# Kernel optimization log

Hardware: AMD Instinct MI355X
Metric: run time of the kernel (lower is better)

Reference implementation:

```python
import jax, jax.numpy as jnp
import numpy as np

B, N, D, H, DK, NREL, TOPK = 32, 49, 512, 8, 64, 14, 14
EPS = 1e-5
SCALE = float(1.0 / np.sqrt(DK))


def _linear(x, W, b):
    return x @ W + b


def _ln(x, g, b):
    m = jnp.mean(x, -1, keepdims=True)
    v = jnp.var(x, -1, keepdims=True)
    return (x - m) * jax.lax.rsqrt(v + EPS) * g + b


def setup_inputs() -> dict:
    key = jax.random.key(0)
    ks = jax.random.split(key, 24)

    def rn(k, shape, s=0.03):
        return (jax.random.normal(k, shape) * s).astype(jnp.float32)

    inp = {}
    inp['queries'] = jax.random.normal(ks[0], (B, N, D), jnp.float32)
    inp['keys'] = jax.random.normal(ks[1], (B, N, D), jnp.float32)
    inp['values'] = jax.random.normal(ks[2], (B, N, D), jnp.float32)
    inp['Wq'] = rn(ks[3], (D, H * DK)); inp['bq'] = jnp.zeros((H * DK,), jnp.float32)
    inp['Wk'] = rn(ks[4], (D, H * DK)); inp['bk'] = jnp.zeros((H * DK,), jnp.float32)
    inp['Wv'] = rn(ks[5], (D, H * DK)); inp['bv'] = jnp.zeros((H * DK,), jnp.float32)
    inp['Wo'] = rn(ks[6], (H * DK, D)); inp['bo'] = jnp.zeros((D,), jnp.float32)
    inp['rel_embed'] = rn(ks[7], (NREL, DK), 0.5)
    inp['Wproj'] = rn(ks[8], (DK, D)); inp['bproj'] = jnp.zeros((D,), jnp.float32)
    inp['Wgate'] = rn(ks[9], (D, 1)); inp['bgate'] = jnp.zeros((1,), jnp.float32)
    inp['Wc1'] = rn(ks[10], (2 * D, 256)); inp['bc1'] = jnp.zeros((256,), jnp.float32)
    inp['gc'] = jnp.ones((256,), jnp.float32); inp['bcln'] = jnp.zeros((256,), jnp.float32)
    inp['Wc2'] = rn(ks[11], (256, NREL)); inp['bc2'] = jnp.zeros((NREL,), jnp.float32)
    inp['Wr1'] = rn(ks[12], (2 * D, D)); inp['br1'] = jnp.zeros((D,), jnp.float32)
    inp['gr'] = jnp.ones((D,), jnp.float32); inp['brln'] = jnp.zeros((D,), jnp.float32)
    inp['Wr2'] = rn(ks[13], (D, D)); inp['br2'] = jnp.zeros((D,), jnp.float32)
    inp['convW'] = rn(ks[14], (D, D, 3, 3)); inp['convb'] = jnp.zeros((D,), jnp.float32)
    return inp


def reference(queries, keys, values, Wq, bq, Wk, bk, Wv, bv, Wo, bo,
              rel_embed, Wproj, bproj, Wgate, bgate,
              Wc1, bc1, gc, bcln, Wc2, bc2,
              Wr1, br1, gr, brln, Wr2, br2, convW, convb):
    Bsz, nq, _ = queries.shape
    # spatial_net: conv3x3 -> BatchNorm2d(affine=False, training stats) -> ReLU
    x = queries.transpose(0, 2, 1).reshape(Bsz, D, 7, 7)
    h = jax.lax.conv_general_dilated(x, convW, (1, 1), ((1, 1), (1, 1)),
                                     dimension_numbers=('NCHW', 'OIHW', 'NCHW'))
    h = h + convb[None, :, None, None]
    mu = jnp.mean(h, (0, 2, 3), keepdims=True)
    var = jnp.var(h, (0, 2, 3), keepdims=True)
    h = jax.nn.relu((h - mu) * jax.lax.rsqrt(var + EPS))
    xs = h.reshape(Bsz, D, nq).transpose(0, 2, 1)  # [B,49,D]
    eq = xs + queries
    ek = xs + keys
    ev = xs + values
    nk = ek.shape[1]
    # multi-head projections
    q = _linear(eq, Wq, bq).reshape(Bsz, nq, H, DK).transpose(0, 2, 1, 3)
    k = _linear(ek, Wk, bk).reshape(Bsz, nk, H, DK).transpose(0, 2, 1, 3)
    v = _linear(ev, Wv, bv).reshape(Bsz, nk, H, DK).transpose(0, 2, 1, 3)
    att = jnp.einsum('bhqd,bhkd->bhqk', q, k) * SCALE
    # pairwise relation features [B,nq,nk,2D]
    pair = jnp.concatenate([
        jnp.broadcast_to(eq[:, :, None, :], (Bsz, nq, nk, D)),
        jnp.broadcast_to(ek[:, None, :, :], (Bsz, nq, nk, D))], -1)
    logits = _linear(jax.nn.relu(_ln(_linear(pair, Wc1, bc1), gc, bcln)), Wc2, bc2)
    probs = jax.nn.softmax(logits, -1)
    tp, ti = jax.lax.top_k(probs, TOPK)
    tp = tp / (jnp.sum(tp, -1, keepdims=True) + 1e-8)
    rel_emb = jnp.sum(tp[..., None] * rel_embed[ti], -2)  # [B,nq,nk,DK]
    proj = _linear(rel_emb, Wproj, bproj)
    rf = _linear(jax.nn.relu(_ln(_linear(pair, Wr1, br1), gr, brln)), Wr2, br2)
    gate = jax.nn.sigmoid(_linear(rf + proj, Wgate, bgate))[..., 0]  # [B,nq,nk]
    enh = att * (1.0 + gate[:, None, :, :])
    w = jax.nn.softmax(enh, -1)
    out = jnp.einsum('bhqk,bhkd->bhqd', w, v).transpose(0, 2, 1, 3).reshape(Bsz, nq, H * DK)
    return _linear(out, Wo, bo)
```

## Files before the change

### kernel.cpp

```cpp
#include <hip/hip_runtime.h>
#include <math.h>

typedef _Float16 f16;
typedef _Float16 f16x2 __attribute__((ext_vector_type(2)));
typedef _Float16 f16x8 __attribute__((ext_vector_type(8)));
typedef float f32x4 __attribute__((ext_vector_type(4)));

static constexpr int Mrows = 1568;
static constexpr int NPAIR = 76832;
static constexpr float SCALEC = 0.125f;
#define EPSV 1e-5f

__device__ inline float wsum(float v) {
#pragma unroll
  for (int m = 32; m >= 1; m >>= 1) v += __shfl_xor(v, m, 64);
  return v;
}
__device__ inline float wmax(float v) {
#pragma unroll
  for (int m = 32; m >= 1; m >>= 1) v = fmaxf(v, __shfl_xor(v, m, 64));
  return v;
}
__device__ inline void gld16(const void* g, void* l) {
  __builtin_amdgcn_global_load_lds((const __attribute__((address_space(1))) void*)g,
                                   (__attribute__((address_space(3))) void*)l, 16, 0, 0);
}
__device__ inline f16x2 H2(unsigned u) { return __builtin_bit_cast(f16x2, u); }
__device__ inline unsigned U32(f16x2 h) { return __builtin_bit_cast(unsigned, h); }
__device__ inline f16x2 pk2(float a, float b) {
  return __builtin_bit_cast(f16x2, __builtin_amdgcn_cvt_pkrtz(a, b));
}
__device__ inline float qsum(float v) {
  v += __shfl_xor(v, 1, 64);
  v += __shfl_xor(v, 2, 64);
  return v;
}

__global__ __launch_bounds__(256) void prep(const float* __restrict__ queries,
                                            const float* __restrict__ convW,
                                            float* __restrict__ h,
                                            f16* __restrict__ Qp,
                                            f16* __restrict__ Wtb) {
  int bx = blockIdx.x;
  int tid = threadIdx.x;
  if (bx < 784) {
    ((float4*)h)[bx * 256 + tid] = make_float4(0.f, 0.f, 0.f, 0.f);
  } else if (bx < 784 + 5184) {
    int idx = (bx - 784) * 256 + tid;
    int c = idx & 511;
    int iijj = (idx >> 9) % 81;
    int b = idx / (81 * 512);
    int ii = iijj / 9, jj = iijj % 9;
    float v = 0.f;
    if (ii >= 1 && ii <= 7 && jj >= 1 && jj <= 7)
      v = queries[(((size_t)(b * 49 + (ii - 1) * 7 + (jj - 1))) << 9) + c];
    Qp[idx] = (f16)v;
  } else {
    int idx = (bx - 5968) * 256 + tid;
    int o = idx >> 9, c = idx & 511;
    const float* s = convW + (size_t)o * 4608 + c * 9;
    f16* d = Wtb + (size_t)o * 4608 + c;
#pragma unroll
    for (int t = 0; t < 9; t++) d[t * 512] = (f16)s[t];
  }
}

__global__ __launch_bounds__(256) void smalls_kernel(
    const float* __restrict__ Wproj, const float* __restrict__ Wgate,
    const float* __restrict__ rel_embed, const float* __restrict__ bproj,
    const float* __restrict__ br2, const float* __restrict__ bgate,
    const float* __restrict__ Wr2, float* __restrict__ crel,
    float* __restrict__ wrg, float* __restrict__ cconst) {
  int tid = threadIdx.x;
  if (blockIdx.x == 0) {
    __shared__ float pg[64];
    if (tid < 64) {
      float s = 0.f;
      for (int d = 0; d < 512; d++) s += Wproj[tid * 512 + d] * Wgate[d];
      pg[tid] = s;
    }
    __syncthreads();
    if (tid < 14) {
      float s = 0.f;
      for (int dk = 0; dk < 64; dk++) s += rel_embed[tid * 64 + dk] * pg[dk];
      crel[tid] = s;
    }
    if (tid == 64) {
      float s = 0.f;
      for (int d = 0; d < 512; d++) s += (bproj[d] + br2[d]) * Wgate[d];
      cconst[0] = s + bgate[0];
    }
  } else {
    int d = (blockIdx.x - 1) * 256 + tid;
    float s = 0.f;
    for (int d2 = 0; d2 < 512; d2++) s += Wr2[(size_t)d * 512 + d2] * Wgate[d2];
    wrg[d] = s;
  }
}

struct TJobs { const float* src[8]; f16* dst[8]; int cols[8]; };
__global__ __launch_bounds__(256) void transpose_w(TJobs tj) {
  int z = blockIdx.z;
  int cols = tj.cols[z];
  int n0 = blockIdx.x * 32;
  if (n0 >= cols) return;
  int k0 = blockIdx.y * 32;
  const float* src = tj.src[z];
  f16* dst = tj.dst[z];
  __shared__ float tile[32][33];
  int tid = threadIdx.x;
  int c = tid & 31, r0 = tid >> 5;
#pragma unroll
  for (int i = 0; i < 4; i++) {
    int r = r0 + i * 8;
    tile[r][c] = src[(size_t)(k0 + r) * cols + n0 + c];
  }
  __syncthreads();
#pragma unroll
  for (int i = 0; i < 4; i++) {
    int r = r0 + i * 8;
    dst[(size_t)(n0 + r) * 512 + k0 + c] = (f16)tile[c][r];
  }
}

struct T2Jobs { const float* src[4]; unsigned* dst[4]; int C[4]; };
__global__ __launch_bounds__(256) void t2h(T2Jobs tj) {
  int z = blockIdx.z;
  int C = tj.C[z];
  int c0 = blockIdx.x * 32;
  if (c0 >= C) return;
  int r0 = blockIdx.y * 32;
  const float* src = tj.src[z];
  unsigned* dst = tj.dst[z];
  __shared__ float tile[32][33];
  int t = threadIdx.x;
  int cc = t & 31, rr = t >> 5;
#pragma unroll
  for (int i = 0; i < 4; i++)
    tile[cc][rr + i * 8] = src[(size_t)(r0 + rr + i * 8) * C + c0 + cc];
  __syncthreads();
  int r = t & 31, cp = t >> 5;
#pragma unroll
  for (int i = 0; i < 2; i++) {
    int c = cp + i * 8;
    f16x2 p = pk2(tile[2 * c][r], tile[2 * c + 1][r]);
    dst[(size_t)((c0 >> 1) + c) * 1568 + r0 + r] = U32(p);
  }
}

__global__ __launch_bounds__(256) void conv_mfma(const f16* __restrict__ Qp,
                                                 const f16* __restrict__ Wtb,
                                                 float* __restrict__ h) {
  __shared__ f16 As2[2048];
  __shared__ f16 Bs2[2048];
  int tid = threadIdx.x;
  int n0 = blockIdx.x * 64;
  int m0 = blockIdx.y * 64;
  int kb = blockIdx.z * 576;
  int lane = tid & 63, wv = tid >> 6;
  int kq = (tid >> 4) & 3, mm = tid & 15;
  int rowA = m0 + wv * 16 + mm;
  if (rowA > Mrows - 1) rowA = Mrows - 1;
  int b = rowA / 49, p = rowA % 49;
  int pi = p / 7, pj = p % 7;
  const f16* qbase = Qp + (size_t)b * 81 * 512 + kq * 8;
  int rowB = n0 + wv * 16 + mm;
  const f16* bSrc = Wtb + (size_t)rowB * 4608 + kq * 8 + kb;
  f16* aDst = &As2[wv * 512];
  f16* bDst = &Bs2[wv * 512];
  f32x4 acc[4];
#pragma unroll
  for (int i = 0; i < 4; i++) acc[i] = (f32x4){0.f, 0.f, 0.f, 0.f};
  for (int s = 0; s < 18; s++) {
    int k0 = kb + s * 32;
    int t = k0 >> 9, c0 = k0 & 511;
    int ti = t / 3, tj = t - ti * 3;
    const f16* aSrc = qbase + (size_t)((pi + ti) * 9 + (pj + tj)) * 512 + c0;
    gld16(aSrc, aDst);
    gld16(bSrc + s * 32, bDst);
    __syncthreads();
    f16x8 a = *(const f16x8*)&As2[(wv << 9) + (lane << 3)];
#pragma unroll
    for (int nb = 0; nb < 4; nb++) {
      f16x8 bf = *(const f16x8*)&Bs2[(nb << 9) + (lane << 3)];
      acc[nb] = __builtin_amdgcn_mfma_f32_16x16x32_f16(a, bf, acc[nb], 0, 0, 0);
    }
    __syncthreads();
  }
  int r0 = m0 + wv * 16 + ((lane >> 4) << 2);
  int cw = lane & 15;
#pragma unroll
  for (int nb = 0; nb < 4; nb++) {
    int col = n0 + nb * 16 + cw;
#pragma unroll
    for (int r = 0; r < 4; r++) {
      int row = r0 + r;
      if (row < Mrows) atomicAdd(&h[(size_t)row * 512 + col], acc[nb][r]);
    }
  }
}

__global__ __launch_bounds__(256) void bn_stats(const float* __restrict__ h,
                                                float* __restrict__ mu,
                                                float* __restrict__ rsg) {
  int c = blockIdx.x;
  int tid = threadIdx.x;
  float s = 0.f, ss = 0.f;
  for (int r = tid; r < Mrows; r += 256) {
    float v = h[(size_t)r * 512 + c];
    s += v;
    ss += v * v;
  }
  s = wsum(s);
  ss = wsum(ss);
  __shared__ float r1[4], r2[4];
  int wave = tid >> 6, lane = tid & 63;
  if (lane == 0) { r1[wave] = s; r2[wave] = ss; }
  __syncthreads();
  if (tid == 0) {
    float S = r1[0] + r1[1] + r1[2] + r1[3];
    float SS = r2[0] + r2[1] + r2[2] + r2[3];
    float m = S / (float)Mrows;
    float var = SS / (float)Mrows - m * m;
    mu[c] = m;
    rsg[c] = rsqrtf(var + EPSV);
  }
}

__global__ __launch_bounds__(256) void fuse_xs(
    const float* __restrict__ h, const float* __restrict__ mu,
    const float* __restrict__ rsg, const float* __restrict__ Q,
    const float* __restrict__ Kin, const float* __restrict__ Vin,
    f16* __restrict__ eqh, f16* __restrict__ ekh, f16* __restrict__ evh) {
  int i = blockIdx.x * 256 + threadIdx.x;
  int c = i & 511;
  float xs = fmaxf((h[i] - mu[c]) * rsg[c], 0.f);
  eqh[i] = (f16)(xs + Q[i]);
  ekh[i] = (f16)(xs + Kin[i]);
  evh[i] = (f16)(xs + Vin[i]);
}

struct MJobs { const f16* A[7]; const f16* BT[7]; const float* bias[7]; float* C[7]; int N[7]; };
__global__ __launch_bounds__(256) void gemm_mf(MJobs jb) {
  int z = blockIdx.z;
  int N = jb.N[z];
  int n0 = blockIdx.x * 64;
  if (n0 >= N) return;
  int m0 = blockIdx.y * 64;
  const f16* A = jb.A[z];
  const f16* BT = jb.BT[z];
  __shared__ f16 As2[2048];
  __shared__ f16 Bs2[2048];
  int tid = threadIdx.x, lane = tid & 63, wv = tid >> 6;
  int kq = (tid >> 4) & 3, mm = tid & 15;
  int rowA = m0 + wv * 16 + mm;
  if (rowA > Mrows - 1) rowA = Mrows - 1;
  const f16* aSrc = A + (size_t)rowA * 512 + kq * 8;
  int rowB = n0 + wv * 16 + mm;
  const f16* bSrc = BT + (size_t)rowB * 512 + kq * 8;
  f16* aDst = &As2[wv * 512];
  f16* bDst = &Bs2[wv * 512];
  f32x4 acc[4];
#pragma unroll
  for (int i = 0; i < 4; i++) acc[i] = (f32x4){0.f, 0.f, 0.f, 0.f};
  for (int s = 0; s < 16; s++) {
    gld16(aSrc + s * 32, aDst);
    gld16(bSrc + s * 32, bDst);
    __syncthreads();
    f16x8 a = *(const f16x8*)&As2[(wv << 9) + (lane << 3)];
#pragma unroll
    for (int nb = 0; nb < 4; nb++) {
      f16x8 bf = *(const f16x8*)&Bs2[(nb << 9) + (lane << 3)];
      acc[nb] = __builtin_amdgcn_mfma_f32_16x16x32_f16(a, bf, acc[nb], 0, 0, 0);
    }
    __syncthreads();
  }
  const float* bias = jb.bias[z];
  float* C = jb.C[z];
  int r0 = m0 + wv * 16 + ((lane >> 4) << 2);
  int cw = lane & 15;
#pragma unroll
  for (int nb = 0; nb < 4; nb++) {
    int col = n0 + nb * 16 + cw;
    float bv = bias ? bias[col] : 0.f;
#pragma unroll
    for (int r = 0; r < 4; r++) {
      int row = r0 + r;
      if (row < Mrows) C[(size_t)row * N + col] = acc[nb][r] + bv;
    }
  }
}

__global__ __launch_bounds__(256) void pair_gate(
    const unsigned* __restrict__ CqT, const unsigned* __restrict__ CkT,
    const unsigned* __restrict__ RqT, const unsigned* __restrict__ RkT,
    const float* __restrict__ Wc2, const float* __restrict__ bc2,
    const float* __restrict__ gc, const float* __restrict__ bcln,
    const float* __restrict__ gr, const float* __restrict__ brln,
    const float* __restrict__ crel, const float* __restrict__ wrg,
    const float* __restrict__ cconstp, float* __restrict__ gfac) {
  __shared__ uint4 sTC[512];
  __shared__ uint4 sTR[256];
  __shared__ float scl[14], sb2[14];
  int tid = threadIdx.x;
  if (tid < 128) {
    int dd = tid;
    unsigned w[16];
    w[0] = U32(pk2(gc[2 * dd], gc[2 * dd + 1]));
    w[1] = U32(pk2(bcln[2 * dd], bcln[2 * dd + 1]));
#pragma unroll
    for (int r = 0; r < 14; r++)
      w[2 + r] = U32(pk2(Wc2[(2 * dd) * 14 + r], Wc2[(2 * dd + 1) * 14 + r]));
#pragma unroll
    for (int j = 0; j < 4; j++)
      sTC[dd * 4 + j] = make_uint4(w[4 * j], w[4 * j + 1], w[4 * j + 2], w[4 * j + 3]);
  }
  {
    int dd = tid;
    sTR[dd] = make_uint4(U32(pk2(gr[2 * dd], gr[2 * dd + 1])),
                         U32(pk2(brln[2 * dd], brln[2 * dd + 1])),
                         U32(pk2(wrg[2 * dd], wrg[2 * dd + 1])), 0u);
  }
  if (tid < 14) { scl[tid] = crel[tid]; sb2[tid] = bc2[tid]; }
  __syncthreads();

  int gidx = blockIdx.x * 256 + tid;
  int pid = gidx >> 2;
  int sub = gidx & 3;
  bool valid = pid < NPAIR;
  int pc = valid ? pid : NPAIR - 1;
  int b = pc / 2401;
  int r2 = pc % 2401;
  int q = r2 / 49, k = r2 % 49;
  int rowq = b * 49 + q, rowk = b * 49 + k;
  const f16x2 one2 = {(f16)1.f, (f16)1.f};
  const f16x2 zero2 = {(f16)0.f, (f16)0.f};

  float s1;
  {
    unsigned zc[32];
    const unsigned* cq = CqT + (size_t)sub * 1568 + rowq;
    const unsigned* ck = CkT + (size_t)sub * 1568 + rowk;
    float s = 0.f, ss = 0.f;
#pragma unroll
    for (int j = 0; j < 32; j++) {
      f16x2 z2 = H2(cq[(size_t)j * 4 * 1568]) + H2(ck[(size_t)j * 4 * 1568]);
      zc[j] = U32(z2);
      s = __builtin_amdgcn_fdot2(z2, one2, s, false);
      ss = __builtin_amdgcn_fdot2(z2, z2, ss, false);
    }
    s = qsum(s);
    ss = qsum(ss);
    float mC = s * (1.f / 256.f);
    float var = ss * (1.f / 256.f) - mC * mC;
    float rsC = rsqrtf(var + EPSV);
    f16x2 nm2 = pk2(-mC, -mC);
    f16x2 rs2 = pk2(rsC, rsC);

    float lg[14];
#pragma unroll
    for (int r = 0; r < 14; r++) lg[r] = 0.f;
#pragma unroll
    for (int j = 0; j < 32; j++) {
      int dd = 4 * j + sub;
      uint4 t0 = sTC[dd * 4 + 0];
      uint4 t1 = sTC[dd * 4 + 1];
      uint4 t2 = sTC[dd * 4 + 2];
      uint4 t3 = sTC[dd * 4 + 3];
      f16x2 z2 = H2(zc[j]);
      f16x2 u2 = (z2 + nm2) * rs2;
      f16x2 h2 = __builtin_elementwise_max(u2 * H2(t0.x) + H2(t0.y), zero2);
      lg[0] = __builtin_amdgcn_fdot2(h2, H2(t0.z), lg[0], false);
      lg[1] = __builtin_amdgcn_fdot2(h2, H2(t0.w), lg[1], false);
      lg[2] = __builtin_amdgcn_fdot2(h2, H2(t1.x), lg[2], false);
      lg[3] = __builtin_amdgcn_fdot2(h2, H2(t1.y), lg[3], false);
      lg[4] = __builtin_amdgcn_fdot2(h2, H2(t1.z), lg[4], false);
      lg[5] = __builtin_amdgcn_fdot2(h2, H2(t1.w), lg[5], false);
      lg[6] = __builtin_amdgcn_fdot2(h2, H2(t2.x), lg[6], false);
      lg[7] = __builtin_amdgcn_fdot2(h2, H2(t2.y), lg[7], false);
      lg[8] = __builtin_amdgcn_fdot2(h2, H2(t2.z), lg[8], false);
      lg[9] = __builtin_amdgcn_fdot2(h2, H2(t2.w), lg[9], false);
      lg[10] = __builtin_amdgcn_fdot2(h2, H2(t3.x), lg[10], false);
      lg[11] = __builtin_amdgcn_fdot2(h2, H2(t3.y), lg[11], false);
      lg[12] = __builtin_amdgcn_fdot2(h2, H2(t3.z), lg[12], false);
      lg[13] = __builtin_amdgcn_fdot2(h2, H2(t3.w), lg[13], false);
    }
#pragma unroll
    for (int r = 0; r < 14; r++) lg[r] = qsum(lg[r]) + sb2[r];

    float mx = lg[0];
#pragma unroll
    for (int r = 1; r < 14; r++) mx = fmaxf(mx, lg[r]);
    float se = 0.f, sc = 0.f;
#pragma unroll
    for (int r = 0; r < 14; r++) {
      float e = __expf(lg[r] - mx);
      se += e;
      sc += e * scl[r];
    }
    s1 = sc / (se * (1.f + 1e-8f));
  }

  float s2v;
  {
    unsigned zr[64];
    const unsigned* rq = RqT + (size_t)sub * 1568 + rowq;
    const unsigned* rk = RkT + (size_t)sub * 1568 + rowk;
    float sR = 0.f, ssR = 0.f;
#pragma unroll
    for (int j = 0; j < 64; j++) {
      f16x2 z2 = H2(rq[(size_t)j * 4 * 1568]) + H2(rk[(size_t)j * 4 * 1568]);
      zr[j] = U32(z2);
      sR = __builtin_amdgcn_fdot2(z2, one2, sR, false);
      ssR = __builtin_amdgcn_fdot2(z2, z2, ssR, false);
    }
    sR = qsum(sR);
    ssR = qsum(ssR);
    float mR = sR * (1.f / 512.f);
    float varR = ssR * (1.f / 512.f) - mR * mR;
    float rsR = rsqrtf(varR + EPSV);
    f16x2 nmR2 = pk2(-mR, -mR);
    f16x2 rsR2 = pk2(rsR, rsR);

    float acc = 0.f;
#pragma unroll
    for (int j = 0; j < 64; j++) {
      int dd = 4 * j + sub;
      uint4 tr = sTR[dd];
      f16x2 z2 = H2(zr[j]);
      f16x2 u2 = (z2 + nmR2) * rsR2;
      f16x2 h2 = __builtin_elementwise_max(u2 * H2(tr.x) + H2(tr.y), zero2);
      acc = __builtin_amdgcn_fdot2(h2, H2(tr.z), acc, false);
    }
    s2v = qsum(acc);
  }

  float gin = s1 + s2v + cconstp[0];
  float gate = 1.f / (1.f + __expf(-gin));
  if (valid && sub == 0) gfac[pid] = 1.f + gate;
}

__global__ __launch_bounds__(256) void attn(const float* __restrict__ qb,
                                            const float* __restrict__ kb,
                                            const float* __restrict__ vb,
                                            const float* __restrict__ gfac,
                                            f16* __restrict__ aoh) {
  int b = blockIdx.x >> 3, h = blockIdx.x & 7;
  __shared__ float Kh[64][65];
  __shared__ float Vh[49][65];
  __shared__ float G[2401];
  int tid = threadIdx.x;
  for (int i = tid; i < 49 * 64; i += 256) {
    int k = i >> 6, d = i & 63;
    size_t off = (((size_t)(b * 49 + k)) << 9) + h * 64 + d;
    Kh[k][d] = kb[off];
    Vh[k][d] = vb[off];
  }
  for (int i = tid; i < 15 * 64; i += 256) {
    Kh[49 + (i >> 6)][i & 63] = 0.f;
  }
  for (int i = tid; i < 2401; i += 256) G[i] = gfac[b * 2401 + i];
  __syncthreads();
  int wave = tid >> 6, lane = tid & 63;
  for (int q = wave; q < 49; q += 4) {
    float qv = qb[(((size_t)(b * 49 + q)) << 9) + h * 64 + lane];
    float dot = 0.f;
#pragma unroll
    for (int d = 0; d < 64; d++) dot += __shfl(qv, d, 64) * Kh[lane][d];
    float enh = (lane < 49) ? dot * SCALEC * G[q * 49 + lane] : -1e30f;
    float mxv = wmax(enh);
    float e = (lane < 49) ? __expf(enh - mxv) : 0.f;
    float ssum = wsum(e);
    float w = e / ssum;
    float out = 0.f;
#pragma unroll
    for (int k = 0; k < 49; k++) out += __shfl(w, k, 64) * Vh[k][lane];
    aoh[(((size_t)(b * 49 + q)) << 9) + h * 64 + lane] = (f16)out;
  }
}

extern "C" void kernel_launch(void* const* d_in, const int* in_sizes, int n_in,
                              void* d_out, int out_size, void* d_ws, size_t ws_size,
                              hipStream_t stream) {
  const float* queries = (const float*)d_in[0];
  const float* keys = (const float*)d_in[1];
  const float* values = (const float*)d_in[2];
  const float* Wq = (const float*)d_in[3];
  const float* bq = (const float*)d_in[4];
  const float* Wk = (const float*)d_in[5];
  const float* bk = (const float*)d_in[6];
  const float* Wv = (const float*)d_in[7];
  const float* bv = (const float*)d_in[8];
  const float* Wo = (const float*)d_in[9];
  const float* bo = (const float*)d_in[10];
  const float* rel_embed = (const float*)d_in[11];
  const float* Wproj = (const float*)d_in[12];
  const float* bproj = (const float*)d_in[13];
  const float* Wgate = (const float*)d_in[14];
  const float* bgate = (const float*)d_in[15];
  const float* Wc1 = (const float*)d_in[16];
  const float* bc1 = (const float*)d_in[17];
  const float* gc = (const float*)d_in[18];
  const float* bcln = (const float*)d_in[19];
  const float* Wc2 = (const float*)d_in[20];
  const float* bc2 = (const float*)d_in[21];
  const float* Wr1 = (const float*)d_in[22];
  const float* br1 = (const float*)d_in[23];
  const float* gr = (const float*)d_in[24];
  const float* brln = (const float*)d_in[25];
  const float* Wr2 = (const float*)d_in[26];
  const float* br2 = (const float*)d_in[27];
  const float* convW = (const float*)d_in[28];

  float* W = (float*)d_ws;
  size_t o = 0;
  f16* Qp = (f16*)(W + o); o += 663552;
  f16* Wtb = (f16*)(W + o); o += 1179648;
  f16* WqT = (f16*)(W + o); o += 131072;
  f16* WkT = (f16*)(W + o); o += 131072;
  f16* WvT = (f16*)(W + o); o += 131072;
  f16* WoT = (f16*)(W + o); o += 131072;
  f16* Wc1aT = (f16*)(W + o); o += 65536;
  f16* Wc1bT = (f16*)(W + o); o += 65536;
  f16* Wr1aT = (f16*)(W + o); o += 131072;
  f16* Wr1bT = (f16*)(W + o); o += 131072;
  float* hbuf = W + o; o += 802816;
  f16* eqh = (f16*)(W + o); o += 401408;
  f16* ekh = (f16*)(W + o); o += 401408;
  f16* evh = (f16*)(W + o); o += 401408;
  float* qbuf = W + o; o += 802816;
  float* kbuf = W + o; o += 802816;
  float* vbuf = W + o; o += 802816;
  float* Cqw = W + o; o += 401408;
  float* Ckw = W + o; o += 401408;
  float* Rqw = W + o; o += 802816;
  float* Rkw = W + o; o += 802816;
  f16* aoh = (f16*)(W + o); o += 200704;
  float* gf = W + o; o += 76832;
  float* mu = W + o; o += 512;
  float* rsg = W + o; o += 512;
  float* crel = W + o; o += 16;
  float* wrg = W + o; o += 512;
  float* ccst = W + o; o += 16;
  unsigned* CqT2 = (unsigned*)(W + o); o += 200704;
  unsigned* CkT2 = (unsigned*)(W + o); o += 200704;
  unsigned* RqT2 = (unsigned*)(W + o); o += 401408;
  unsigned* RkT2 = (unsigned*)(W + o); o += 401408;

  hipLaunchKernelGGL(prep, dim3(784 + 5184 + 1024), dim3(256), 0, stream,
                     queries, convW, hbuf, Qp, Wtb);
  hipLaunchKernelGGL(smalls_kernel, dim3(3), dim3(256), 0, stream, Wproj, Wgate,
                     rel_embed, bproj, br2, bgate, Wr2, crel, wrg, ccst);

  TJobs tj;
  tj.src[0] = Wq;  tj.dst[0] = WqT;  tj.cols[0] = 512;
  tj.src[1] = Wk;  tj.dst[1] = WkT;  tj.cols[1] = 512;
  tj.src[2] = Wv;  tj.dst[2] = WvT;  tj.cols[2] = 512;
  tj.src[3] = Wo;  tj.dst[3] = WoT;  tj.cols[3] = 512;
  tj.src[4] = Wc1;             tj.dst[4] = Wc1aT; tj.cols[4] = 256;
  tj.src[5] = Wc1 + 512 * 256; tj.dst[5] = Wc1bT; tj.cols[5] = 256;
  tj.src[6] = Wr1;             tj.dst[6] = Wr1aT; tj.cols[6] = 512;
  tj.src[7] = Wr1 + 512 * 512; tj.dst[7] = Wr1bT; tj.cols[7] = 512;
  hipLaunchKernelGGL(transpose_w, dim3(16, 16, 8), dim3(256), 0, stream, tj);

  hipLaunchKernelGGL(conv_mfma, dim3(8, 25, 8), dim3(256), 0, stream, Qp, Wtb, hbuf);
  hipLaunchKernelGGL(bn_stats, dim3(512), dim3(256), 0, stream, hbuf, mu, rsg);
  hipLaunchKernelGGL(fuse_xs, dim3(3136), dim3(256), 0, stream, hbuf, mu, rsg,
                     queries, keys, values, eqh, ekh, evh);

  MJobs jb;
  jb.A[0] = eqh; jb.BT[0] = WqT;   jb.bias[0] = bq;      jb.C[0] = qbuf; jb.N[0] = 512;
  jb.A[1] = ekh; jb.BT[1] = WkT;   jb.bias[1] = bk;      jb.C[1] = kbuf; jb.N[1] = 512;
  jb.A[2] = evh; jb.BT[2] = WvT;   jb.bias[2] = bv;      jb.C[2] = vbuf; jb.N[2] = 512;
  jb.A[3] = eqh; jb.BT[3] = Wc1aT; jb.bias[3] = bc1;     jb.C[3] = Cqw;  jb.N[3] = 256;
  jb.A[4] = ekh; jb.BT[4] = Wc1bT; jb.bias[4] = nullptr; jb.C[4] = Ckw;  jb.N[4] = 256;
  jb.A[5] = eqh; jb.BT[5] = Wr1aT; jb.bias[5] = br1;     jb.C[5] = Rqw;  jb.N[5] = 512;
  jb.A[6] = ekh; jb.BT[6] = Wr1bT; jb.bias[6] = nullptr; jb.C[6] = Rkw;  jb.N[6] = 512;
  hipLaunchKernelGGL(gemm_mf, dim3(8, 25, 7), dim3(256), 0, stream, jb);

  T2Jobs t2;
  t2.src[0] = Cqw; t2.dst[0] = CqT2; t2.C[0] = 256;
  t2.src[1] = Ckw; t2.dst[1] = CkT2; t2.C[1] = 256;
  t2.src[2] = Rqw; t2.dst[2] = RqT2; t2.C[2] = 512;
  t2.src[3] = Rkw; t2.dst[3] = RkT2; t2.C[3] = 512;
  hipLaunchKernelGGL(t2h, dim3(16, 49, 4), dim3(256), 0, stream, t2);

  hipLaunchKernelGGL(pair_gate, dim3((NPAIR * 4 + 255) / 256), dim3(256), 0, stream,
                     CqT2, CkT2, RqT2, RkT2, Wc2, bc2, gc, bcln, gr, brln, crel,
                     wrg, ccst, gf);
  hipLaunchKernelGGL(attn, dim3(256), dim3(256), 0, stream, qbuf, kbuf, vbuf, gf, aoh);

  MJobs j2;
  j2.A[0] = aoh; j2.BT[0] = WoT; j2.bias[0] = bo; j2.C[0] = (float*)d_out; j2.N[0] = 512;
  for (int z = 1; z < 7; z++) {
    j2.A[z] = nullptr; j2.BT[z] = nullptr; j2.bias[z] = nullptr; j2.C[z] = nullptr; j2.N[z] = 0;
  }
  hipLaunchKernelGGL(gemm_mf, dim3(8, 25, 1), dim3(256), 0, stream, j2);
}
```

Baseline: 358.2 us.

## Decompose pairwise LayerNorm stats into row sums plus per-batch Gram matmuls

The pairwise LayerNorm mean and variance over (Cq+Ck) are now computed algebraically from per-row sums, per-row sums of squares, and a 2*Cq·Ck cross term. The cross term comes from a new per-batch MFMA Gram kernel, and the row sums come from a separate kernel. This removes the first pass over the pair features in pair_gate and the large register buffers that pass needed, lowering register pressure. In exchange it adds two kernels, f16 copies of the GEMM outputs, and the one-pass variance formula with f16-rounded cross terms, which risks cancellation error. smalls_kernel is also rewritten to use wavefront reductions across more blocks.

```diff
diff --git a/kernel.cpp b/kernel.cpp
--- a/kernel.cpp
+++ b/kernel.cpp
@@ -72,12 +72,20 @@
     const float* __restrict__ Wr2, float* __restrict__ crel,
     float* __restrict__ wrg, float* __restrict__ cconst) {
   int tid = threadIdx.x;
+  int wv = tid >> 6, lane = tid & 63;
   if (blockIdx.x == 0) {
     __shared__ float pg[64];
-    if (tid < 64) {
+    for (int o = wv; o < 64; o += 4) {
       float s = 0.f;
-      for (int d = 0; d < 512; d++) s += Wproj[tid * 512 + d] * Wgate[d];
-      pg[tid] = s;
+      for (int d = lane; d < 512; d += 64) s += Wproj[o * 512 + d] * Wgate[d];
+      s = wsum(s);
+      if (lane == 0) pg[o] = s;
+    }
+    if (wv == 3) {
+      float s = 0.f;
+      for (int d = lane; d < 512; d += 64) s += (bproj[d] + br2[d]) * Wgate[d];
+      s = wsum(s);
+      if (lane == 0) cconst[0] = s + bgate[0];
     }
     __syncthreads();
     if (tid < 14) {
@@ -85,16 +93,12 @@
       for (int dk = 0; dk < 64; dk++) s += rel_embed[tid * 64 + dk] * pg[dk];
       crel[tid] = s;
     }
-    if (tid == 64) {
-      float s = 0.f;
-      for (int d = 0; d < 512; d++) s += (bproj[d] + br2[d]) * Wgate[d];
-      cconst[0] = s + bgate[0];
-    }
   } else {
-    int d = (blockIdx.x - 1) * 256 + tid;
+    int d = (blockIdx.x - 1) * 4 + wv;
     float s = 0.f;
-    for (int d2 = 0; d2 < 512; d2++) s += Wr2[(size_t)d * 512 + d2] * Wgate[d2];
-    wrg[d] = s;
+    for (int d2 = lane; d2 < 512; d2 += 64) s += Wr2[(size_t)d * 512 + d2] * Wgate[d2];
+    s = wsum(s);
+    if (lane == 0) wrg[d] = s;
   }
 }
 
@@ -145,6 +149,79 @@
     int c = cp + i * 8;
     f16x2 p = pk2(tile[2 * c][r], tile[2 * c + 1][r]);
     dst[(size_t)((c0 >> 1) + c) * 1568 + r0 + r] = U32(p);
+  }
+}
+
+struct RSJobs { const float* src[4]; int w[4]; };
+__global__ __launch_bounds__(256) void row_sums(RSJobs rj, float* __restrict__ Ssum,
+                                                float* __restrict__ SSsum) {
+  int j = blockIdx.y;
+  int w = rj.w[j];
+  const float* src = rj.src[j];
+  int row = blockIdx.x * 4 + (threadIdx.x >> 6);
+  int lane = threadIdx.x & 63;
+  float s = 0.f, ss = 0.f;
+  for (int c = lane; c < w; c += 64) {
+    float v = src[(size_t)row * w + c];
+    s += v;
+    ss += v * v;
+  }
+  s = wsum(s);
+  ss = wsum(ss);
+  if (lane == 0) {
+    Ssum[j * 1568 + row] = s;
+    SSsum[j * 1568 + row] = ss;
+  }
+}
+
+__global__ __launch_bounds__(256) void gram_mfma(const f16* __restrict__ Cqh,
+                                                 const f16* __restrict__ Ckh,
+                                                 const f16* __restrict__ Rqh,
+                                                 const f16* __restrict__ Rkh,
+                                                 float* __restrict__ dotC,
+                                                 float* __restrict__ dotR) {
+  int idx = blockIdx.x;
+  int z = idx >> 5, b = idx & 31;
+  int K = z ? 512 : 256;
+  const f16* A = (z ? Rqh : Cqh) + (size_t)b * 49 * K;
+  const f16* BT = (z ? Rkh : Ckh) + (size_t)b * 49 * K;
+  float* out = (z ? dotR : dotC) + (size_t)b * 2401;
+  __shared__ f16 As2[2048];
+  __shared__ f16 Bs2[2048];
+  int tid = threadIdx.x, lane = tid & 63, wv = tid >> 6;
+  int kq = (tid >> 4) & 3, mm = tid & 15;
+  int rowA = wv * 16 + mm;
+  if (rowA > 48) rowA = 48;
+  const f16* aSrc = A + (size_t)rowA * K + kq * 8;
+  const f16* bSrc = BT + (size_t)rowA * K + kq * 8;
+  f16* aDst = &As2[wv * 512];
+  f16* bDst = &Bs2[wv * 512];
+  f32x4 acc[4];
+#pragma unroll
+  for (int i = 0; i < 4; i++) acc[i] = (f32x4){0.f, 0.f, 0.f, 0.f};
+  int steps = K >> 5;
+  for (int s = 0; s < steps; s++) {
+    gld16(aSrc + s * 32, aDst);
+    gld16(bSrc + s * 32, bDst);
+    __syncthreads();
+    f16x8 a = *(const f16x8*)&As2[(wv << 9) + (lane << 3)];
+#pragma unroll
+    for (int nb = 0; nb < 4; nb++) {
+      f16x8 bf = *(const f16x8*)&Bs2[(nb << 9) + (lane << 3)];
+      acc[nb] = __builtin_amdgcn_mfma_f32_16x16x32_f16(a, bf, acc[nb], 0, 0, 0);
+    }
+    __syncthreads();
+  }
+  int r0 = wv * 16 + ((lane >> 4) << 2);
+  int cw = lane & 15;
+#pragma unroll
+  for (int nb = 0; nb < 4; nb++) {
+    int col = nb * 16 + cw;
+#pragma unroll
+    for (int r = 0; r < 4; r++) {
+      int row = r0 + r;
+      if (row < 49 && col < 49) out[row * 49 + col] = 2.f * acc[nb][r];
+    }
   }
 }
 
@@ -240,7 +317,10 @@
   evh[i] = (f16)(xs + Vin[i]);
 }
 
-struct MJobs { const f16* A[7]; const f16* BT[7]; const float* bias[7]; float* C[7]; int N[7]; };
+struct MJobs {
+  const f16* A[7]; const f16* BT[7]; const float* bias[7];
+  float* C[7]; f16* Ch[7]; int N[7];
+};
 __global__ __launch_bounds__(256) void gemm_mf(MJobs jb) {
   int z = blockIdx.z;
   int N = jb.N[z];
@@ -277,6 +357,7 @@
   }
   const float* bias = jb.bias[z];
   float* C = jb.C[z];
+  f16* Ch = jb.Ch[z];
   int r0 = m0 + wv * 16 + ((lane >> 4) << 2);
   int cw = lane & 15;
 #pragma unroll
@@ -286,7 +367,11 @@
 #pragma unroll
     for (int r = 0; r < 4; r++) {
       int row = r0 + r;
-      if (row < Mrows) C[(size_t)row * N + col] = acc[nb][r] + bv;
+      if (row < Mrows) {
+        float v = acc[nb][r] + bv;
+        C[(size_t)row * N + col] = v;
+        if (Ch) Ch[(size_t)row * N + col] = (f16)v;
+      }
     }
   }
 }
@@ -298,7 +383,9 @@
     const float* __restrict__ gc, const float* __restrict__ bcln,
     const float* __restrict__ gr, const float* __restrict__ brln,
     const float* __restrict__ crel, const float* __restrict__ wrg,
-    const float* __restrict__ cconstp, float* __restrict__ gfac) {
+    const float* __restrict__ cconstp, const float* __restrict__ Ssum,
+    const float* __restrict__ SSsum, const float* __restrict__ dotC,
+    const float* __restrict__ dotR, float* __restrict__ gfac) {
   __shared__ uint4 sTC[512];
   __shared__ uint4 sTR[256];
   __shared__ float scl[14], sb2[14];
@@ -333,26 +420,14 @@
   int r2 = pc % 2401;
   int q = r2 / 49, k = r2 % 49;
   int rowq = b * 49 + q, rowk = b * 49 + k;
-  const f16x2 one2 = {(f16)1.f, (f16)1.f};
   const f16x2 zero2 = {(f16)0.f, (f16)0.f};
 
   float s1;
   {
-    unsigned zc[32];
-    const unsigned* cq = CqT + (size_t)sub * 1568 + rowq;
-    const unsigned* ck = CkT + (size_t)sub * 1568 + rowk;
-    float s = 0.f, ss = 0.f;
-#pragma unroll
-    for (int j = 0; j < 32; j++) {
-      f16x2 z2 = H2(cq[(size_t)j * 4 * 1568]) + H2(ck[(size_t)j * 4 * 1568]);
-      zc[j] = U32(z2);
-      s = __builtin_amdgcn_fdot2(z2, one2, s, false);
-      ss = __builtin_amdgcn_fdot2(z2, z2, ss, false);
-    }
-    s = qsum(s);
-    ss = qsum(ss);
-    float mC = s * (1.f / 256.f);
-    float var = ss * (1.f / 256.f) - mC * mC;
+    float sC = Ssum[rowq] + Ssum[1568 + rowk];
+    float ssC = SSsum[rowq] + SSsum[1568 + rowk] + dotC[pc];
+    float mC = sC * (1.f / 256.f);
+    float var = ssC * (1.f / 256.f) - mC * mC;
     float rsC = rsqrtf(var + EPSV);
     f16x2 nm2 = pk2(-mC, -mC);
     f16x2 rs2 = pk2(rsC, rsC);
@@ -360,6 +435,8 @@
     float lg[14];
 #pragma unroll
     for (int r = 0; r < 14; r++) lg[r] = 0.f;
+    const unsigned* cq = CqT + (size_t)sub * 1568 + rowq;
+    const unsigned* ck = CkT + (size_t)sub * 1568 + rowk;
 #pragma unroll
     for (int j = 0; j < 32; j++) {
       int dd = 4 * j + sub;
@@ -367,7 +444,7 @@
       uint4 t1 = sTC[dd * 4 + 1];
       uint4 t2 = sTC[dd * 4 + 2];
       uint4 t3 = sTC[dd * 4 + 3];
-      f16x2 z2 = H2(zc[j]);
+      f16x2 z2 = H2(cq[(size_t)j * 4 * 1568]) + H2(ck[(size_t)j * 4 * 1568]);
       f16x2 u2 = (z2 + nm2) * rs2;
       f16x2 h2 = __builtin_elementwise_max(u2 * H2(t0.x) + H2(t0.y), zero2);
       lg[0] = __builtin_amdgcn_fdot2(h2, H2(t0.z), lg[0], false);
@@ -403,19 +480,8 @@
 
   float s2v;
   {
-    unsigned zr[64];
-    const unsigned* rq = RqT + (size_t)sub * 1568 + rowq;
-    const unsigned* rk = RkT + (size_t)sub * 1568 + rowk;
-    float sR = 0.f, ssR = 0.f;
-#pragma unroll
-    for (int j = 0; j < 64; j++) {
-      f16x2 z2 = H2(rq[(size_t)j * 4 * 1568]) + H2(rk[(size_t)j * 4 * 1568]);
-      zr[j] = U32(z2);
-      sR = __builtin_amdgcn_fdot2(z2, one2, sR, false);
-      ssR = __builtin_amdgcn_fdot2(z2, z2, ssR, false);
-    }
-    sR = qsum(sR);
-    ssR = qsum(ssR);
+    float sR = Ssum[2 * 1568 + rowq] + Ssum[3 * 1568 + rowk];
+    float ssR = SSsum[2 * 1568 + rowq] + SSsum[3 * 1568 + rowk] + dotR[pc];
     float mR = sR * (1.f / 512.f);
     float varR = ssR * (1.f / 512.f) - mR * mR;
     float rsR = rsqrtf(varR + EPSV);
@@ -423,11 +489,13 @@
     f16x2 rsR2 = pk2(rsR, rsR);
 
     float acc = 0.f;
+    const unsigned* rq = RqT + (size_t)sub * 1568 + rowq;
+    const unsigned* rk = RkT + (size_t)sub * 1568 + rowk;
 #pragma unroll
     for (int j = 0; j < 64; j++) {
       int dd = 4 * j + sub;
       uint4 tr = sTR[dd];
-      f16x2 z2 = H2(zr[j]);
+      f16x2 z2 = H2(rq[(size_t)j * 4 * 1568]) + H2(rk[(size_t)j * 4 * 1568]);
       f16x2 u2 = (z2 + nmR2) * rsR2;
       f16x2 h2 = __builtin_elementwise_max(u2 * H2(tr.x) + H2(tr.y), zero2);
       acc = __builtin_amdgcn_fdot2(h2, H2(tr.z), acc, false);
@@ -546,10 +614,18 @@
   unsigned* CkT2 = (unsigned*)(W + o); o += 200704;
   unsigned* RqT2 = (unsigned*)(W + o); o += 401408;
   unsigned* RkT2 = (unsigned*)(W + o); o += 401408;
+  f16* Cqh = (f16*)(W + o); o += 200704;
+  f16* Ckh = (f16*)(W + o); o += 200704;
+  f16* Rqh = (f16*)(W + o); o += 401408;
+  f16* Rkh = (f16*)(W + o); o += 401408;
+  float* Ssum = W + o; o += 6272;
+  float* SSsum = W + o; o += 6272;
+  float* dotC = W + o; o += 76832;
+  float* dotR = W + o; o += 76832;
 
   hipLaunchKernelGGL(prep, dim3(784 + 5184 + 1024), dim3(256), 0, stream,
                      queries, convW, hbuf, Qp, Wtb);
-  hipLaunchKernelGGL(smalls_kernel, dim3(3), dim3(256), 0, stream, Wproj, Wgate,
+  hipLaunchKernelGGL(smalls_kernel, dim3(129), dim3(256), 0, stream, Wproj, Wgate,
                      rel_embed, bproj, br2, bgate, Wr2, crel, wrg, ccst);
 
   TJobs tj;
@@ -569,14 +645,22 @@
                      queries, keys, values, eqh, ekh, evh);
 
   MJobs jb;
+  for (int z = 0; z < 7; z++) jb.Ch[z] = nullptr;
   jb.A[0] = eqh; jb.BT[0] = WqT;   jb.bias[0] = bq;      jb.C[0] = qbuf; jb.N[0] = 512;
   jb.A[1] = ekh; jb.BT[1] = WkT;   jb.bias[1] = bk;      jb.C[1] = kbuf; jb.N[1] = 512;
   jb.A[2] = evh; jb.BT[2] = WvT;   jb.bias[2] = bv;      jb.C[2] = vbuf; jb.N[2] = 512;
-  jb.A[3] = eqh; jb.BT[3] = Wc1aT; jb.bias[3] = bc1;     jb.C[3] = Cqw;  jb.N[3] = 256;
-  jb.A[4] = ekh; jb.BT[4] = Wc1bT; jb.bias[4] = nullptr; jb.C[4] = Ckw;  jb.N[4] = 256;
-  jb.A[5] = eqh; jb.BT[5] = Wr1aT; jb.bias[5] = br1;     jb.C[5] = Rqw;  jb.N[5] = 512;
-  jb.A[6] = ekh; jb.BT[6] = Wr1bT; jb.bias[6] = nullptr; jb.C[6] = Rkw;  jb.N[6] = 512;
+  jb.A[3] = eqh; jb.BT[3] = Wc1aT; jb.bias[3] = bc1;     jb.C[3] = Cqw;  jb.N[3] = 256; jb.Ch[3] = Cqh;
+  jb.A[4] = ekh; jb.BT[4] = Wc1bT; jb.bias[4] = nullptr; jb.C[4] = Ckw;  jb.N[4] = 256; jb.Ch[4] = Ckh;
+  jb.A[5] = eqh; jb.BT[5] = Wr1aT; jb.bias[5] = br1;     jb.C[5] = Rqw;  jb.N[5] = 512; jb.Ch[5] = Rqh;
+  jb.A[6] = ekh; jb.BT[6] = Wr1bT; jb.bias[6] = nullptr; jb.C[6] = Rkw;  jb.N[6] = 512; jb.Ch[6] = Rkh;
   hipLaunchKernelGGL(gemm_mf, dim3(8, 25, 7), dim3(256), 0, stream, jb);
+
+  RSJobs rj;
+  rj.src[0] = Cqw; rj.w[0] = 256;
+  rj.src[1] = Ckw; rj.w[1] = 256;
+  rj.src[2] = Rqw; rj.w[2] = 512;
+  rj.src[3] = Rkw; rj.w[3] = 512;
+  hipLaunchKernelGGL(row_sums, dim3(392, 4), dim3(256), 0, stream, rj, Ssum, SSsum);
 
   T2Jobs t2;
   t2.src[0] = Cqw; t2.dst[0] = CqT2; t2.C[0] = 256;
@@ -585,15 +669,19 @@
   t2.src[3] = Rkw; t2.dst[3] = RkT2; t2.C[3] = 512;
   hipLaunchKernelGGL(t2h, dim3(16, 49, 4), dim3(256), 0, stream, t2);
 
+  hipLaunchKernelGGL(gram_mfma, dim3(64), dim3(256), 0, stream, Cqh, Ckh, Rqh, Rkh,
+                     dotC, dotR);
+
   hipLaunchKernelGGL(pair_gate, dim3((NPAIR * 4 + 255) / 256), dim3(256), 0, stream,
                      CqT2, CkT2, RqT2, RkT2, Wc2, bc2, gc, bcln, gr, brln, crel,
-                     wrg, ccst, gf);
+                     wrg, ccst, Ssum, SSsum, dotC, dotR, gf);
   hipLaunchKernelGGL(attn, dim3(256), dim3(256), 0, stream, qbuf, kbuf, vbuf, gf, aoh);
 
   MJobs j2;
+  for (int z = 0; z < 7; z++) {
+    j2.A[z] = nullptr; j2.BT[z] = nullptr; j2.bias[z] = nullptr;
+    j2.C[z] = nullptr; j2.Ch[z] = nullptr; j2.N[z] = 0;
+  }
   j2.A[0] = aoh; j2.BT[0] = WoT; j2.bias[0] = bo; j2.C[0] = (float*)d_out; j2.N[0] = 512;
-  for (int z = 1; z < 7; z++) {
-    j2.A[z] = nullptr; j2.BT[z] = nullptr; j2.bias[z] = nullptr; j2.C[z] = nullptr; j2.N[z] = 0;
-  }
   hipLaunchKernelGGL(gemm_mf, dim3(8, 25, 1), dim3(256), 0, stream, j2);
 }
```

After: 359.9 us. No clear change (+0.5%).
